# Performance work log

Measured on AMD Instinct MI355X. Metric: run time of the kernel, lower is better.

Reference implementation:

```python
import jax, jax.numpy as jnp
import numpy as np

HEADS = 4
LEAKY_SLOPE = 0.2  # PyG GATConv default negative_slope


def gat_layer(x, src, dst, W, a_src, a_dst, b):
    """One PyG-style GATConv (concat=True). x:[N,F_in], W:[F_in,H*C]."""
    N = x.shape[0]
    h = (x @ W).reshape(N, HEADS, -1)                    # [N,H,C]
    alpha_src = jnp.sum(h * a_src, axis=-1)              # [N,H]
    alpha_dst = jnp.sum(h * a_dst, axis=-1)              # [N,H]
    e = jax.nn.leaky_relu(alpha_src[src] + alpha_dst[dst], LEAKY_SLOPE)  # [E,H]
    # numerically stable softmax over edges grouped by destination node
    emax = jax.ops.segment_max(e, dst, num_segments=N)   # [N,H]
    emax = jnp.where(jnp.isfinite(emax), emax, 0.0)
    ex = jnp.exp(e - emax[dst])                          # [E,H]
    denom = jax.ops.segment_sum(ex, dst, num_segments=N) # [N,H]
    alpha = ex / (denom[dst] + 1e-16)                    # [E,H]
    out = jax.ops.segment_sum(h[src] * alpha[:, :, None], dst, num_segments=N)  # [N,H,C]
    return out.reshape(N, -1) + b


def setup_inputs() -> dict:
    key = jax.random.key(0)
    ks = jax.random.split(key, 10)
    N, E = 100000, 1600000
    IN, HID, OUT = 128, 128, 128
    c1, c2 = HID // HEADS, OUT // HEADS
    x = jax.random.normal(ks[0], (N, IN), jnp.float32)
    edge_index = jax.random.randint(ks[1], (2, E), 0, N, jnp.int32)
    s_in, s_h = 1.0 / np.sqrt(IN), 1.0 / np.sqrt(HID)
    W1 = jax.random.normal(ks[2], (IN, HEADS * c1), jnp.float32) * s_in
    a_src1 = jax.random.normal(ks[3], (HEADS, c1), jnp.float32) * 0.1
    a_dst1 = jax.random.normal(ks[4], (HEADS, c1), jnp.float32) * 0.1
    b1 = jnp.zeros((HEADS * c1,), jnp.float32)
    W2 = jax.random.normal(ks[5], (HID, HEADS * c2), jnp.float32) * s_h
    a_src2 = jax.random.normal(ks[6], (HEADS, c2), jnp.float32) * 0.1
    a_dst2 = jax.random.normal(ks[7], (HEADS, c2), jnp.float32) * 0.1
    b2 = jnp.zeros((HEADS * c2,), jnp.float32)
    return {"x": x, "edge_index": edge_index, "W1": W1, "a_src1": a_src1,
            "a_dst1": a_dst1, "b1": b1, "W2": W2, "a_src2": a_src2,
            "a_dst2": a_dst2, "b2": b2}


def reference(x, edge_index, W1, a_src1, a_dst1, b1, W2, a_src2, a_dst2, b2):
    N = x.shape[0]
    # PyG GATConv default: add self-loops
    loop = jnp.arange(N, dtype=edge_index.dtype)
    src = jnp.concatenate([edge_index[0], loop])
    dst = jnp.concatenate([edge_index[1], loop])
    h = gat_layer(x, src, dst, W1, a_src1, a_dst1, b1)
    h = jax.nn.elu(h)  # ELU between layers
    out = gat_layer(h, src, dst, W2, a_src2, a_dst2, b2)
    per_head = jnp.split(out, HEADS, axis=-1)
    return (out, *per_head)
```

## Files before the change

kernel.cpp:

```cpp
#include <hip/hip_runtime.h>
#include <hip/hip_fp16.h>
#include <cstddef>
#include <cstdint>

#define LEAKY 0.2f
#define CAP   64
#define BKSH  7
#define BKN   128
#define SUBC  8
#define SCAP  512

__device__ __forceinline__ float lrelu(float x) {
    return x > 0.f ? x : LEAKY * x;
}

#define GROWS 64
__global__ __launch_bounds__(256) void gemm128_k(const float* __restrict__ A,
                                                 const float* __restrict__ Wg,
                                                 const float* __restrict__ a_s,
                                                 const float* __restrict__ a_d,
                                                 __half* __restrict__ H,
                                                 float* __restrict__ asrc,
                                                 float* __restrict__ adst, int M)
{
    __shared__ float As[GROWS][129];
    int t  = threadIdx.x;
    int r0 = blockIdx.x * GROWS;

#pragma unroll
    for (int i = 0; i < 8; ++i) {
        int f   = t + i * 256;
        int row = f >> 5;
        int k4  = (f & 31) * 4;
        int gr  = r0 + row;
        if (gr >= M) gr = M - 1;
        float4 v = *(const float4*)(A + (size_t)gr * 128 + k4);
        As[row][k4 + 0] = v.x;
        As[row][k4 + 1] = v.y;
        As[row][k4 + 2] = v.z;
        As[row][k4 + 3] = v.w;
    }
    __syncthreads();

    int row = t & 63;
    int cg  = __builtin_amdgcn_readfirstlane(t >> 6);
    const float* __restrict__ wbase = Wg + cg * 32;

    float acc[32];
#pragma unroll
    for (int j = 0; j < 32; ++j) acc[j] = 0.f;

#pragma unroll 2
    for (int k = 0; k < 128; ++k) {
        float a = As[row][k];
        const float* __restrict__ wr = wbase + k * 128;
#pragma unroll
        for (int j = 0; j < 32; ++j)
            acc[j] += a * wr[j];
    }

    int gr = r0 + row;
    if (gr < M) {
        __half hv[32];
#pragma unroll
        for (int j = 0; j < 32; ++j) hv[j] = __float2half(acc[j]);
        float4* o = (float4*)((char*)H + (size_t)gr * 256 + cg * 64);
#pragma unroll
        for (int j4 = 0; j4 < 4; ++j4)
            o[j4] = ((const float4*)hv)[j4];

        float ps = 0.f, pd = 0.f;
#pragma unroll
        for (int j = 0; j < 32; ++j) {
            ps += acc[j] * a_s[cg * 32 + j];
            pd += acc[j] * a_d[cg * 32 + j];
        }
        asrc[(size_t)gr * 4 + cg] = ps;
        adst[(size_t)gr * 4 + cg] = pd;
    }
}

__global__ __launch_bounds__(256) void gemm_build_k(
    const float* __restrict__ A, const float* __restrict__ Wg,
    const float* __restrict__ a_s, const float* __restrict__ a_d,
    __half* __restrict__ H, float* __restrict__ asrc,
    float* __restrict__ adst, int M,
    const int* __restrict__ srcv, const int* __restrict__ dstv, int E, int EPB,
    int* __restrict__ bcur, uint2* __restrict__ bpair)
{
    __shared__ float As[GROWS][129];
    int t  = threadIdx.x;
    int r0 = blockIdx.x * GROWS;
    int cls = blockIdx.x & (SUBC - 1);

    int ebase = blockIdx.x * EPB;
    int ne = E - ebase;
    if (ne > EPB) ne = EPB;
    int d[4], s[4];
#pragma unroll
    for (int i = 0; i < 4; ++i) {
        int idx = t + i * 256;
        bool ok = idx < ne;
        int e = ebase + idx;
        d[i] = ok ? dstv[ok ? e : 0] : -1;
        s[i] = ok ? srcv[ok ? e : 0] : 0;
    }

#pragma unroll
    for (int i = 0; i < 8; ++i) {
        int f   = t + i * 256;
        int row = f >> 5;
        int k4  = (f & 31) * 4;
        int gr  = r0 + row;
        if (gr >= M) gr = M - 1;
        float4 v = *(const float4*)(A + (size_t)gr * 128 + k4);
        As[row][k4 + 0] = v.x;
        As[row][k4 + 1] = v.y;
        As[row][k4 + 2] = v.z;
        As[row][k4 + 3] = v.w;
    }
    __syncthreads();

    int r[4];
#pragma unroll
    for (int i = 0; i < 4; ++i) {
        int q = (d[i] >> BKSH) * SUBC + cls;
        r[i] = (d[i] >= 0) ? atomicAdd(&bcur[q], 1) : 0;
    }

    int row = t & 63;
    int cg  = __builtin_amdgcn_readfirstlane(t >> 6);
    const float* __restrict__ wbase = Wg + cg * 32;

    float acc[32];
#pragma unroll
    for (int j = 0; j < 32; ++j) acc[j] = 0.f;

#pragma unroll 2
    for (int k = 0; k < 128; ++k) {
        float a = As[row][k];
        const float* __restrict__ wr = wbase + k * 128;
#pragma unroll
        for (int j = 0; j < 32; ++j)
            acc[j] += a * wr[j];
    }

#pragma unroll
    for (int i = 0; i < 4; ++i) {
        if (d[i] >= 0 && r[i] < SCAP) {
            int q = (d[i] >> BKSH) * SUBC + cls;
            bpair[(size_t)q * SCAP + r[i]] =
                make_uint2((unsigned)s[i], (unsigned)d[i]);
        }
    }

    int gr = r0 + row;
    if (gr < M) {
        __half hv[32];
#pragma unroll
        for (int j = 0; j < 32; ++j) hv[j] = __float2half(acc[j]);
        float4* o = (float4*)((char*)H + (size_t)gr * 256 + cg * 64);
#pragma unroll
        for (int j4 = 0; j4 < 4; ++j4)
            o[j4] = ((const float4*)hv)[j4];

        float ps = 0.f, pd = 0.f;
#pragma unroll
        for (int j = 0; j < 32; ++j) {
            ps += acc[j] * a_s[cg * 32 + j];
            pd += acc[j] * a_d[cg * 32 + j];
        }
        asrc[(size_t)gr * 4 + cg] = ps;
        adst[(size_t)gr * 4 + cg] = pd;
    }
}

__global__ __launch_bounds__(256) void bin_scatter_k(
    const int* __restrict__ bcur, const uint2* __restrict__ bpair,
    int* __restrict__ cnt, int* __restrict__ adjp, int N)
{
    __shared__ int cntL[BKN];
    __shared__ int adjL[BKN * CAP];

    int b = blockIdx.x;
    int t = threadIdx.x;
    if (t < BKN) cntL[t] = 0;
    __syncthreads();

#pragma unroll 1
    for (int c = 0; c < SUBC; ++c) {
        int q = b * SUBC + c;
        int m = bcur[q];
        if (m > SCAP) m = SCAP;
        const uint2* __restrict__ bp = bpair + (size_t)q * SCAP;
        for (int i = t; i < m; i += 256) {
            uint2 pr = bp[i];
            int ln = (int)(pr.y & (BKN - 1));
            int r = atomicAdd(&cntL[ln], 1);
            if (r < CAP) adjL[(ln << 6) + r] = (int)pr.x;
        }
    }
    __syncthreads();

    int4* __restrict__ dst4 = (int4*)(adjp + (size_t)b * BKN * CAP);
    const int4* __restrict__ src4 = (const int4*)adjL;
#pragma unroll
    for (int i = 0; i < BKN * CAP / 4 / 256; ++i)
        dst4[t + i * 256] = src4[t + i * 256];
    if (t < BKN) {
        int n = b * BKN + t;
        if (n < N) cnt[n] = cntL[t];
    }
}

__global__ __launch_bounds__(256) void aggregate_k(
    const int* __restrict__ cnt_g, const int* __restrict__ adjp,
    const __half* __restrict__ h, const float* __restrict__ asrc,
    const float* __restrict__ adst, const float* __restrict__ bias,
    float* __restrict__ out, int N, int final_flag)
{
    __shared__ float    s_w[4][CAP][4];
    __shared__ unsigned s_off[4][CAP];

    int wv = __builtin_amdgcn_readfirstlane(threadIdx.x >> 6);
    int l  = threadIdx.x & 63;
    int n  = blockIdx.x * 4 + wv;
    if (n >= N) return;
    int hd = l >> 4;
    int sl = l & 15;

    int cnt = cnt_g[n];
    if (cnt > CAP) cnt = CAP;

    float4 ad4 = ((const float4*)adst)[n];
    float4 as4 = ((const float4*)asrc)[n];
    float e_self = lrelu(((const float*)&as4)[hd] + ((const float*)&ad4)[hd]);

    const char* __restrict__ hb = (const char*)h;
    unsigned l4 = (unsigned)l * 4u;

    if (l < cnt) {
        int s = adjp[(size_t)n * CAP + l];
        s_off[wv][l] = (unsigned)s << 8;
        float4 a4 = ((const float4*)asrc)[s];
        float4 wl;
        wl.x = lrelu(a4.x + ad4.x);
        wl.y = lrelu(a4.y + ad4.y);
        wl.z = lrelu(a4.z + ad4.z);
        wl.w = lrelu(a4.w + ad4.w);
        *(float4*)&s_w[wv][l][0] = wl;
    }
    asm volatile("s_waitcnt lgkmcnt(0)" ::: "memory");
    __builtin_amdgcn_wave_barrier();

    float m = e_self;
    for (int j = sl; j < cnt; j += 16)
        m = fmaxf(m, s_w[wv][j][hd]);
#pragma unroll
    for (int mk = 8; mk > 0; mk >>= 1)
        m = fmaxf(m, __shfl_xor(m, mk, 64));

    float ws = 0.f;
    for (int j = sl; j < cnt; j += 16) {
        float w = __expf(s_w[wv][j][hd] - m);
        s_w[wv][j][hd] = w;
        ws += w;
    }
#pragma unroll
    for (int mk = 8; mk > 0; mk >>= 1)
        ws += __shfl_xor(ws, mk, 64);
    float wself = __expf(e_self - m);
    float ssum  = ws + wself;

    asm volatile("s_waitcnt lgkmcnt(0)" ::: "memory");
    __builtin_amdgcn_wave_barrier();

    float2 acc;
    {
        __half2 hv = *(const __half2*)(hb + ((size_t)n << 8) + l4);
        float2 f = __half22float2(hv);
        acc.x = wself * f.x;
        acc.y = wself * f.y;
    }
#pragma unroll 4
    for (int j = 0; j < cnt; ++j) {
        float w = s_w[wv][j][hd];
        unsigned off = s_off[wv][j] + l4;
        __half2 hv = *(const __half2*)(hb + off);
        float2 f = __half22float2(hv);
        acc.x = fmaf(w, f.x, acc.x);
        acc.y = fmaf(w, f.y, acc.y);
    }

    float inv = 1.f / (ssum + 1e-16f);
    float2 bv = *(const float2*)(bias + 2 * l);
    float v0 = acc.x * inv + bv.x;
    float v1 = acc.y * inv + bv.y;
    if (final_flag) {
        *(float2*)(out + (size_t)n * 128 + 2 * l) = make_float2(v0, v1);
        *(float2*)(out + (size_t)N * 128 + (size_t)hd * N * 32
                   + (size_t)n * 32 + 2 * sl) = make_float2(v0, v1);
    } else {
        v0 = v0 > 0.f ? v0 : expm1f(v0);
        v1 = v1 > 0.f ? v1 : expm1f(v1);
        *(float2*)(out + (size_t)n * 128 + 2 * l) = make_float2(v0, v1);
    }
}

extern "C" void kernel_launch(void* const* d_in, const int* in_sizes, int n_in,
                              void* d_out, int out_size, void* d_ws, size_t ws_size,
                              hipStream_t stream)
{
    const float* x   = (const float*)d_in[0];
    const int*   ei  = (const int*)d_in[1];
    const float* W1  = (const float*)d_in[2];
    const float* aS1 = (const float*)d_in[3];
    const float* aD1 = (const float*)d_in[4];
    const float* b1  = (const float*)d_in[5];
    const float* W2  = (const float*)d_in[6];
    const float* aS2 = (const float*)d_in[7];
    const float* aD2 = (const float*)d_in[8];
    const float* b2  = (const float*)d_in[9];
    float* out = (float*)d_out;

    int N = in_sizes[0] / 128;
    int E = in_sizes[1] / 2;
    const int* srcv = ei;
    const int* dstv = ei + E;

    char* p = (char*)d_ws;
    auto alloc = [&](size_t bytes) {
        char* r = p;
        p += (bytes + 255) & ~(size_t)255;
        return r;
    };
    int NBK = (N + BKN - 1) >> BKSH;
    __half* h    = (__half*)alloc((size_t)N * 128 * 2);
    float* x2     = (float*)alloc((size_t)N * 128 * 4);
    float* asrc   = (float*)alloc((size_t)N * 4 * 4);
    float* adst   = (float*)alloc((size_t)N * 4 * 4);
    int*   cnt    = (int*)alloc((size_t)N * 4);
    int*   adjp   = (int*)alloc((size_t)NBK * BKN * CAP * 4);
    int*   bcur   = (int*)alloc((size_t)NBK * SUBC * 4);
    uint2* bpair  = (uint2*)alloc((size_t)NBK * SUBC * SCAP * 8);

    hipMemsetAsync(bcur, 0, (size_t)NBK * SUBC * 4, stream);

    int gemm_grid = (N + GROWS - 1) / GROWS;
    int EPB       = (E + gemm_grid - 1) / gemm_grid;
    int agg_grid  = (N + 3) / 4;

    gemm_build_k<<<gemm_grid, 256, 0, stream>>>(
        x, W1, aS1, aD1, h, asrc, adst, N, srcv, dstv, E, EPB, bcur, bpair);
    bin_scatter_k<<<NBK, 256, 0, stream>>>(bcur, bpair, cnt, adjp, N);
    aggregate_k<<<agg_grid, 256, 0, stream>>>(cnt, adjp, h, asrc, adst, b1, x2, N, 0);

    gemm128_k<<<gemm_grid, 256, 0, stream>>>(x2, W2, aS2, aD2, h, asrc, adst, N);
    aggregate_k<<<agg_grid, 256, 0, stream>>>(cnt, adjp, h, asrc, adst, b2, out, N, 1);
}
```

Measured before the change: 526.3 us.

## Gather 16-byte feature chunks for four edges per wave in aggregation

After: 503.8 us. 4.3% less time.

```diff
diff --git a/kernel.cpp b/kernel.cpp
--- a/kernel.cpp
+++ b/kernel.cpp
@@ -226,18 +226,18 @@
     int l  = threadIdx.x & 63;
     int n  = blockIdx.x * 4 + wv;
     if (n >= N) return;
-    int hd = l >> 4;
-    int sl = l & 15;
+    int g  = l >> 4;
+    int q  = l & 15;
+    int hq = q >> 2;
 
     int cnt = cnt_g[n];
     if (cnt > CAP) cnt = CAP;
 
     float4 ad4 = ((const float4*)adst)[n];
     float4 as4 = ((const float4*)asrc)[n];
-    float e_self = lrelu(((const float*)&as4)[hd] + ((const float*)&ad4)[hd]);
+    float e_self = lrelu(((const float*)&as4)[g] + ((const float*)&ad4)[g]);
 
     const char* __restrict__ hb = (const char*)h;
-    unsigned l4 = (unsigned)l * 4u;
 
     if (l < cnt) {
         int s = adjp[(size_t)n * CAP + l];
@@ -254,16 +254,16 @@
     __builtin_amdgcn_wave_barrier();
 
     float m = e_self;
-    for (int j = sl; j < cnt; j += 16)
-        m = fmaxf(m, s_w[wv][j][hd]);
+    for (int j = q; j < cnt; j += 16)
+        m = fmaxf(m, s_w[wv][j][g]);
 #pragma unroll
     for (int mk = 8; mk > 0; mk >>= 1)
         m = fmaxf(m, __shfl_xor(m, mk, 64));
 
     float ws = 0.f;
-    for (int j = sl; j < cnt; j += 16) {
-        float w = __expf(s_w[wv][j][hd] - m);
-        s_w[wv][j][hd] = w;
+    for (int j = q; j < cnt; j += 16) {
+        float w = __expf(s_w[wv][j][g] - m);
+        s_w[wv][j][g] = w;
         ws += w;
     }
 #pragma unroll
@@ -275,35 +275,70 @@
     asm volatile("s_waitcnt lgkmcnt(0)" ::: "memory");
     __builtin_amdgcn_wave_barrier();
 
-    float2 acc;
+    float inv  = 1.f / (ssum + 1e-16f);
+    float invh = __shfl(inv,   hq << 4, 64);
+    float wsh  = __shfl(wself, hq << 4, 64);
+
+    unsigned qoff    = (unsigned)q * 16u;
+    unsigned selfoff = ((unsigned)n << 8) + qoff;
+    float acc[8];
     {
-        __half2 hv = *(const __half2*)(hb + ((size_t)n << 8) + l4);
-        float2 f = __half22float2(hv);
-        acc.x = wself * f.x;
-        acc.y = wself * f.y;
-    }
-#pragma unroll 4
-    for (int j = 0; j < cnt; ++j) {
-        float w = s_w[wv][j][hd];
-        unsigned off = s_off[wv][j] + l4;
-        __half2 hv = *(const __half2*)(hb + off);
-        float2 f = __half22float2(hv);
-        acc.x = fmaf(w, f.x, acc.x);
-        acc.y = fmaf(w, f.y, acc.y);
-    }
-
-    float inv = 1.f / (ssum + 1e-16f);
-    float2 bv = *(const float2*)(bias + 2 * l);
-    float v0 = acc.x * inv + bv.x;
-    float v1 = acc.y * inv + bv.y;
-    if (final_flag) {
-        *(float2*)(out + (size_t)n * 128 + 2 * l) = make_float2(v0, v1);
-        *(float2*)(out + (size_t)N * 128 + (size_t)hd * N * 32
-                   + (size_t)n * 32 + 2 * sl) = make_float2(v0, v1);
-    } else {
-        v0 = v0 > 0.f ? v0 : expm1f(v0);
-        v1 = v1 > 0.f ? v1 : expm1f(v1);
-        *(float2*)(out + (size_t)n * 128 + 2 * l) = make_float2(v0, v1);
+        float4 raw = *(const float4*)(hb + selfoff);
+        const __half2* hp = (const __half2*)&raw;
+        float sw = (g == 0) ? wsh : 0.f;
+#pragma unroll
+        for (int i = 0; i < 4; ++i) {
+            float2 f = __half22float2(hp[i]);
+            acc[2 * i]     = sw * f.x;
+            acc[2 * i + 1] = sw * f.y;
+        }
+    }
+
+#pragma unroll 2
+    for (int j = 0; j < cnt; j += 4) {
+        int e = j + g;
+        bool v = e < cnt;
+        float w = v ? s_w[wv][e][hq] : 0.f;
+        unsigned off = (v ? s_off[wv][e] : ((unsigned)n << 8)) + qoff;
+        float4 raw = *(const float4*)(hb + off);
+        const __half2* hp = (const __half2*)&raw;
+#pragma unroll
+        for (int i = 0; i < 4; ++i) {
+            float2 f = __half22float2(hp[i]);
+            acc[2 * i]     = fmaf(w, f.x, acc[2 * i]);
+            acc[2 * i + 1] = fmaf(w, f.y, acc[2 * i + 1]);
+        }
+    }
+
+#pragma unroll
+    for (int i = 0; i < 8; ++i) {
+        acc[i] += __shfl_xor(acc[i], 16, 64);
+        acc[i] += __shfl_xor(acc[i], 32, 64);
+    }
+
+    if (g == 0) {
+        float o8[8];
+        const float* bq = bias + 8 * q;
+#pragma unroll
+        for (int i = 0; i < 8; ++i)
+            o8[i] = acc[i] * invh + bq[i];
+        if (final_flag) {
+            float4* o = (float4*)(out + (size_t)n * 128 + 8 * q);
+            o[0] = ((const float4*)o8)[0];
+            o[1] = ((const float4*)o8)[1];
+            int ch = (8 * q) & 31;
+            float4* o2 = (float4*)(out + (size_t)N * 128
+                          + (size_t)hq * N * 32 + (size_t)n * 32 + ch);
+            o2[0] = ((const float4*)o8)[0];
+            o2[1] = ((const float4*)o8)[1];
+        } else {
+#pragma unroll
+            for (int i = 0; i < 8; ++i)
+                o8[i] = o8[i] > 0.f ? o8[i] : expm1f(o8[i]);
+            float4* o = (float4*)(out + (size_t)n * 128 + 8 * q);
+            o[0] = ((const float4*)o8)[0];
+            o[1] = ((const float4*)o8)[1];
+        }
     }
 }
 
```
